# Optimization experiments

Measured on AMD Instinct MI355X. Metric: run time of the kernel, lower is better.

Reference implementation:

```python
import jax, jax.numpy as jnp
import numpy as np

EMBED = 1024
HEADS = 16
HDIM = 64
FFN = 4 * EMBED
EPS = 1e-5


def setup_inputs() -> dict:
    key = jax.random.key(0)
    ks = jax.random.split(key, 12)
    def lin(k, fan_in, shape):
        b = 1.0 / np.sqrt(fan_in)
        return jax.random.uniform(k, shape, jnp.float32, -b, b)
    return {
        "x": jax.random.normal(ks[0], (4, 2048, EMBED), jnp.float32),
        "Wq": lin(ks[1], EMBED, (EMBED, HEADS * HDIM)),
        "Wk": lin(ks[2], EMBED, (EMBED, HEADS * HDIM)),
        "Wv": lin(ks[3], EMBED, (EMBED, HEADS * HDIM)),
        "Wo": lin(ks[4], HEADS * HDIM, (HEADS * HDIM, EMBED)),
        "ln1_g": jnp.ones((EMBED,), jnp.float32),
        "ln1_b": jnp.zeros((EMBED,), jnp.float32),
        "ln2_g": jnp.ones((EMBED,), jnp.float32),
        "ln2_b": jnp.zeros((EMBED,), jnp.float32),
        "W1": lin(ks[5], EMBED, (EMBED, FFN)),
        "b1": lin(ks[6], EMBED, (FFN,)),
        "W2": lin(ks[7], FFN, (FFN, EMBED)),
        "b2": lin(ks[8], FFN, (EMBED,)),
    }


def _layer_norm(x, g, b):
    mu = jnp.mean(x, axis=-1, keepdims=True)
    var = jnp.var(x, axis=-1, keepdims=True)
    return (x - mu) * jax.lax.rsqrt(var + EPS) * g + b


def reference(x, Wq, Wk, Wv, Wo, ln1_g, ln1_b, ln2_g, ln2_b, W1, b1, W2, b2):
    B, S, _ = x.shape
    residual = x
    h = _layer_norm(x, ln1_g, ln1_b)
    # project and split heads: [B, H, S, Dh]
    q = (h @ Wq).reshape(B, S, HEADS, HDIM).transpose(0, 2, 1, 3)
    k = (h @ Wk).reshape(B, S, HEADS, HDIM).transpose(0, 2, 1, 3)
    v = (h @ Wv).reshape(B, S, HEADS, HDIM).transpose(0, 2, 1, 3)
    scale = HDIM ** -0.5
    scores = jnp.einsum("bhqd,bhkd->bhqk", q, k) * scale
    # causal mask (upper triangle excluded above diagonal -> -inf)
    mask = jnp.triu(jnp.ones((S, S), bool), k=1)
    scores = jnp.where(mask, -jnp.inf, scores)
    attn = jax.nn.softmax(scores, axis=-1)
    out = jnp.einsum("bhqk,bhkd->bhqd", attn, v)
    out = out.transpose(0, 2, 1, 3).reshape(B, S, HEADS * HDIM)
    x = residual + out @ Wo
    residual = x
    h = _layer_norm(x, ln2_g, ln2_b)
    h = jax.nn.gelu(h @ W1 + b1, approximate=False) @ W2 + b2
    return residual + h
```

## Files before the change

kernel.cpp:

```cpp
#include <hip/hip_runtime.h>
#include <hip/hip_bf16.h>
#include <math.h>

typedef __bf16 bf16;
typedef bf16 bf16x8 __attribute__((ext_vector_type(8)));
typedef bf16 bf16x4 __attribute__((ext_vector_type(4)));
typedef float f32x4 __attribute__((ext_vector_type(4)));

#define ROWS 8192
#define EMB  1024
#define NH   16
#define HD   64
#define FFN  4096
#define QKVN 3072
#define SEQ  2048

__device__ __forceinline__ void gl2lds16(const bf16* g, bf16* l) {
  __builtin_amdgcn_global_load_lds((const __attribute__((address_space(1))) void*)g,
                                   (__attribute__((address_space(3))) void*)l, 16, 0, 0);
}

__global__ void transpose_cast(const float* __restrict__ W, bf16* __restrict__ Wt,
                               int K, int N, float scale) {
  __shared__ float tile[32][33];
  const int n0 = blockIdx.x * 32, k0 = blockIdx.y * 32;
  const int tx = threadIdx.x & 31, ty = threadIdx.x >> 5;
#pragma unroll
  for (int i = 0; i < 32; i += 8)
    tile[ty + i][tx] = W[(size_t)(k0 + ty + i) * N + n0 + tx];
  __syncthreads();
#pragma unroll
  for (int i = 0; i < 32; i += 8)
    Wt[(size_t)(n0 + ty + i) * K + k0 + tx] = (bf16)(tile[tx][ty + i] * scale);
}

__global__ void v_transpose(const bf16* __restrict__ qkv, bf16* __restrict__ vt) {
  __shared__ bf16 tile[32][33];
  const int s0 = blockIdx.x * 32, d0 = blockIdx.y * 32, bh = blockIdx.z;
  const int b = bh >> 4, h = bh & 15;
  const int tx = threadIdx.x & 31, ty = threadIdx.x >> 5;
#pragma unroll
  for (int i = 0; i < 32; i += 8)
    tile[ty + i][tx] = qkv[(size_t)(b * SEQ + s0 + ty + i) * QKVN + 2 * EMB + h * HD + d0 + tx];
  __syncthreads();
#pragma unroll
  for (int i = 0; i < 32; i += 8)
    vt[(size_t)(bh * HD + d0 + ty + i) * SEQ + s0 + tx] = tile[tx][ty + i];
}

__global__ void layernorm_bf16(const float* __restrict__ x, const float* __restrict__ g,
                               const float* __restrict__ b, bf16* __restrict__ out) {
  const int row = blockIdx.x;
  const int t = threadIdx.x;
  const float4 v = ((const float4*)(x + (size_t)row * EMB))[t];
  float s = v.x + v.y + v.z + v.w;
  float ss = v.x * v.x + v.y * v.y + v.z * v.z + v.w * v.w;
#pragma unroll
  for (int off = 32; off; off >>= 1) {
    s += __shfl_down(s, off);
    ss += __shfl_down(ss, off);
  }
  __shared__ float sbuf[8];
  const int wave = t >> 6, lane = t & 63;
  if (lane == 0) { sbuf[wave] = s; sbuf[4 + wave] = ss; }
  __syncthreads();
  if (t == 0) {
    float S = sbuf[0] + sbuf[1] + sbuf[2] + sbuf[3];
    float SS = sbuf[4] + sbuf[5] + sbuf[6] + sbuf[7];
    float mu = S * (1.0f / EMB);
    float var = SS * (1.0f / EMB) - mu * mu;
    sbuf[0] = mu;
    sbuf[1] = rsqrtf(var + 1e-5f);
  }
  __syncthreads();
  const float mu = sbuf[0], rs = sbuf[1];
  const float4 gv = ((const float4*)g)[t];
  const float4 bv = ((const float4*)b)[t];
  bf16x4 o;
  o[0] = (bf16)((v.x - mu) * rs * gv.x + bv.x);
  o[1] = (bf16)((v.y - mu) * rs * gv.y + bv.y);
  o[2] = (bf16)((v.z - mu) * rs * gv.z + bv.z);
  o[3] = (bf16)((v.w - mu) * rs * gv.w + bv.w);
  *(bf16x4*)(out + (size_t)row * EMB + t * 4) = o;
}

template <int EPI>
__global__ __launch_bounds__(256, 2) void gemm_bt(
    const bf16* __restrict__ A, const bf16* __restrict__ Bt, void* __restrict__ C,
    int M, int N, int K, const float* __restrict__ bias, const float* __restrict__ resid) {
  __shared__ __align__(16) bf16 As[128 * 32];
  __shared__ __align__(16) bf16 Bs[128 * 32];
  const int tid = threadIdx.x;
  const int lane = tid & 63;
  const int wave = tid >> 6;
  const int wm = (wave >> 1) * 64;
  const int wn = (wave & 1) * 64;
  const int m0 = blockIdx.y * 128;
  const int n0 = blockIdx.x * 128;
  const int quad = lane >> 4;
  const int l16 = lane & 15;
  const int k0 = quad * 8;
  const int srow = wave * 32;
  const int lrow = lane >> 2;
  const int lcol = (lane & 3) * 8;

  f32x4 acc[4][4] = {};

  for (int kt = 0; kt < K; kt += 32) {
    __syncthreads();
    gl2lds16(A + (size_t)(m0 + srow + lrow) * K + kt + lcol, &As[srow * 32]);
    gl2lds16(A + (size_t)(m0 + srow + 16 + lrow) * K + kt + lcol, &As[(srow + 16) * 32]);
    gl2lds16(Bt + (size_t)(n0 + srow + lrow) * K + kt + lcol, &Bs[srow * 32]);
    gl2lds16(Bt + (size_t)(n0 + srow + 16 + lrow) * K + kt + lcol, &Bs[(srow + 16) * 32]);
    __syncthreads();
    bf16x8 af[4], bfr[4];
#pragma unroll
    for (int i = 0; i < 4; i++) af[i] = *(const bf16x8*)&As[(wm + i * 16 + l16) * 32 + k0];
#pragma unroll
    for (int j = 0; j < 4; j++) bfr[j] = *(const bf16x8*)&Bs[(wn + j * 16 + l16) * 32 + k0];
#pragma unroll
    for (int i = 0; i < 4; i++)
#pragma unroll
      for (int j = 0; j < 4; j++)
        acc[i][j] = __builtin_amdgcn_mfma_f32_16x16x32_bf16(af[i], bfr[j], acc[i][j], 0, 0, 0);
  }

#pragma unroll
  for (int i = 0; i < 4; i++)
#pragma unroll
    for (int j = 0; j < 4; j++)
#pragma unroll
      for (int r = 0; r < 4; r++) {
        const int row = m0 + wm + i * 16 + quad * 4 + r;
        const int col = n0 + wn + j * 16 + l16;
        const size_t idx = (size_t)row * N + col;
        float v = acc[i][j][r];
        if (EPI == 0) {
          ((bf16*)C)[idx] = (bf16)v;
        } else if (EPI == 1) {
          ((float*)C)[idx] = v + resid[idx];
        } else if (EPI == 2) {
          v += bias[col];
          v = 0.5f * v * (1.0f + erff(v * 0.70710678118654752f));
          ((bf16*)C)[idx] = (bf16)v;
        } else {
          ((float*)C)[idx] = v + bias[col] + resid[idx];
        }
      }
}

__global__ __launch_bounds__(256, 4) void flash_attn(
    const bf16* __restrict__ qkv, const bf16* __restrict__ vt, bf16* __restrict__ out) {
  const int pr = blockIdx.x;
  const int bh = blockIdx.y;
  const int b = bh >> 4, h = bh & 15;
  const int tid = threadIdx.x;
  const int lane = tid & 63, wave = tid >> 6;
  const int quad = lane >> 4, l16 = lane & 15;

  __shared__ __align__(16) bf16 Ks[64][72];
  __shared__ __align__(16) bf16 Vts[64][72];
  __shared__ __align__(16) bf16 Ps[4][16][72];

  const size_t rowbase = (size_t)b * SEQ;
  const int srow = tid >> 3;
  const int sc8 = (tid & 7) * 8;
  const bf16* kbase = qkv + rowbase * QKVN + EMB + h * HD;
  const bf16* vbase = vt + (size_t)(bh * HD) * SEQ;

#pragma unroll 1
  for (int half = 0; half < 2; half++) {
    const int qt = half ? pr : 31 - pr;
    const int qrow_a = qt * 64 + wave * 16 + l16;
    const bf16* qptr = qkv + (rowbase + qrow_a) * QKVN + h * HD;
    const bf16x8 qf0 = *(const bf16x8*)(qptr + quad * 8);
    const bf16x8 qf1 = *(const bf16x8*)(qptr + 32 + quad * 8);
    f32x4 o0 = {}, o1 = {}, o2 = {}, o3 = {};
    f32x4 lsum = {};
    const int qrow_c = qt * 64 + wave * 16 + quad * 4;

#pragma unroll 1
    for (int kt = 0; kt <= qt; kt++) {
      __syncthreads();
      *(bf16x8*)&Ks[srow][sc8] =
          *(const bf16x8*)(kbase + (size_t)(kt * 64 + srow) * QKVN + sc8);
      *(bf16x8*)&Ks[srow + 32][sc8] =
          *(const bf16x8*)(kbase + (size_t)(kt * 64 + srow + 32) * QKVN + sc8);
      *(bf16x8*)&Vts[srow][sc8] =
          *(const bf16x8*)(vbase + (size_t)srow * SEQ + kt * 64 + sc8);
      *(bf16x8*)&Vts[srow + 32][sc8] =
          *(const bf16x8*)(vbase + (size_t)(srow + 32) * SEQ + kt * 64 + sc8);
      __syncthreads();

      if (kt < qt) {
#pragma unroll
        for (int j = 0; j < 4; j++) {
          const bf16x8 kf0 = *(const bf16x8*)&Ks[j * 16 + l16][quad * 8];
          const bf16x8 kf1 = *(const bf16x8*)&Ks[j * 16 + l16][32 + quad * 8];
          f32x4 a = {};
          a = __builtin_amdgcn_mfma_f32_16x16x32_bf16(qf0, kf0, a, 0, 0, 0);
          a = __builtin_amdgcn_mfma_f32_16x16x32_bf16(qf1, kf1, a, 0, 0, 0);
#pragma unroll
          for (int r = 0; r < 4; r++) {
            const float pj = __expf(a[r]);
            lsum[r] += pj;
            Ps[wave][quad * 4 + r][j * 16 + l16] = (bf16)pj;
          }
        }
      } else {
#pragma unroll
        for (int j = 0; j < 4; j++) {
          if (j > wave) {
#pragma unroll
            for (int r = 0; r < 4; r++)
              Ps[wave][quad * 4 + r][j * 16 + l16] = (bf16)0.0f;
          } else {
            const bf16x8 kf0 = *(const bf16x8*)&Ks[j * 16 + l16][quad * 8];
            const bf16x8 kf1 = *(const bf16x8*)&Ks[j * 16 + l16][32 + quad * 8];
            f32x4 a = {};
            a = __builtin_amdgcn_mfma_f32_16x16x32_bf16(qf0, kf0, a, 0, 0, 0);
            a = __builtin_amdgcn_mfma_f32_16x16x32_bf16(qf1, kf1, a, 0, 0, 0);
            if (j == wave) {
#pragma unroll
              for (int r = 0; r < 4; r++) {
                const float v = (l16 > quad * 4 + r) ? -INFINITY : a[r];
                const float pj = __expf(v);
                lsum[r] += pj;
                Ps[wave][quad * 4 + r][j * 16 + l16] = (bf16)pj;
              }
            } else {
#pragma unroll
              for (int r = 0; r < 4; r++) {
                const float pj = __expf(a[r]);
                lsum[r] += pj;
                Ps[wave][quad * 4 + r][j * 16 + l16] = (bf16)pj;
              }
            }
          }
        }
      }

      const bf16x8 af0 = *(const bf16x8*)&Ps[wave][l16][quad * 8];
      const bf16x8 af1 = *(const bf16x8*)&Ps[wave][l16][32 + quad * 8];
      {
        const bf16x8 vf0 = *(const bf16x8*)&Vts[0 + l16][quad * 8];
        const bf16x8 vf1 = *(const bf16x8*)&Vts[0 + l16][32 + quad * 8];
        o0 = __builtin_amdgcn_mfma_f32_16x16x32_bf16(af0, vf0, o0, 0, 0, 0);
        o0 = __builtin_amdgcn_mfma_f32_16x16x32_bf16(af1, vf1, o0, 0, 0, 0);
      }
      {
        const bf16x8 vf0 = *(const bf16x8*)&Vts[16 + l16][quad * 8];
        const bf16x8 vf1 = *(const bf16x8*)&Vts[16 + l16][32 + quad * 8];
        o1 = __builtin_amdgcn_mfma_f32_16x16x32_bf16(af0, vf0, o1, 0, 0, 0);
        o1 = __builtin_amdgcn_mfma_f32_16x16x32_bf16(af1, vf1, o1, 0, 0, 0);
      }
      {
        const bf16x8 vf0 = *(const bf16x8*)&Vts[32 + l16][quad * 8];
        const bf16x8 vf1 = *(const bf16x8*)&Vts[32 + l16][32 + quad * 8];
        o2 = __builtin_amdgcn_mfma_f32_16x16x32_bf16(af0, vf0, o2, 0, 0, 0);
        o2 = __builtin_amdgcn_mfma_f32_16x16x32_bf16(af1, vf1, o2, 0, 0, 0);
      }
      {
        const bf16x8 vf0 = *(const bf16x8*)&Vts[48 + l16][quad * 8];
        const bf16x8 vf1 = *(const bf16x8*)&Vts[48 + l16][32 + quad * 8];
        o3 = __builtin_amdgcn_mfma_f32_16x16x32_bf16(af0, vf0, o3, 0, 0, 0);
        o3 = __builtin_amdgcn_mfma_f32_16x16x32_bf16(af1, vf1, o3, 0, 0, 0);
      }
    }

#pragma unroll
    for (int r = 0; r < 4; r++) {
      float ls = lsum[r];
      ls += __shfl_xor(ls, 1);
      ls += __shfl_xor(ls, 2);
      ls += __shfl_xor(ls, 4);
      ls += __shfl_xor(ls, 8);
      const float iv = 1.0f / ls;
      bf16* op = out + (rowbase + qrow_c + r) * EMB + h * HD;
      op[0 + l16] = (bf16)(o0[r] * iv);
      op[16 + l16] = (bf16)(o1[r] * iv);
      op[32 + l16] = (bf16)(o2[r] * iv);
      op[48 + l16] = (bf16)(o3[r] * iv);
    }
  }
}

extern "C" void kernel_launch(void* const* d_in, const int* in_sizes, int n_in,
                              void* d_out, int out_size, void* d_ws, size_t ws_size,
                              hipStream_t stream) {
  const float* x     = (const float*)d_in[0];
  const float* Wq    = (const float*)d_in[1];
  const float* Wk    = (const float*)d_in[2];
  const float* Wv    = (const float*)d_in[3];
  const float* Wo    = (const float*)d_in[4];
  const float* ln1_g = (const float*)d_in[5];
  const float* ln1_b = (const float*)d_in[6];
  const float* ln2_g = (const float*)d_in[7];
  const float* ln2_b = (const float*)d_in[8];
  const float* W1    = (const float*)d_in[9];
  const float* b1    = (const float*)d_in[10];
  const float* W2    = (const float*)d_in[11];
  const float* b2    = (const float*)d_in[12];
  float* out = (float*)d_out;

  bf16* p = (bf16*)d_ws;
  bf16* wqkv_t = p;                 p += (size_t)QKVN * EMB;
  bf16* wo_t   = p;                 p += (size_t)EMB * EMB;
  bf16* w1_t   = p;                 p += (size_t)FFN * EMB;
  bf16* w2_t   = p;                 p += (size_t)EMB * FFN;
  bf16* h      = p;                 p += (size_t)ROWS * EMB;
  bf16* qkv    = p;                 p += (size_t)ROWS * QKVN;
  bf16* attn_o = p;                 p += (size_t)ROWS * EMB;
  bf16* ffn1   = p;
  bf16* vt     = h;

  transpose_cast<<<dim3(32, 32), 256, 0, stream>>>(Wq, wqkv_t, EMB, EMB, 0.125f);
  transpose_cast<<<dim3(32, 32), 256, 0, stream>>>(Wk, wqkv_t + (size_t)EMB * EMB, EMB, EMB, 1.0f);
  transpose_cast<<<dim3(32, 32), 256, 0, stream>>>(Wv, wqkv_t + (size_t)2 * EMB * EMB, EMB, EMB, 1.0f);
  transpose_cast<<<dim3(32, 32), 256, 0, stream>>>(Wo, wo_t, EMB, EMB, 1.0f);
  transpose_cast<<<dim3(128, 32), 256, 0, stream>>>(W1, w1_t, EMB, FFN, 1.0f);
  transpose_cast<<<dim3(32, 128), 256, 0, stream>>>(W2, w2_t, FFN, EMB, 1.0f);

  layernorm_bf16<<<ROWS, 256, 0, stream>>>(x, ln1_g, ln1_b, h);

  gemm_bt<0><<<dim3(QKVN / 128, ROWS / 128), 256, 0, stream>>>(
      h, wqkv_t, qkv, ROWS, QKVN, EMB, nullptr, nullptr);

  v_transpose<<<dim3(SEQ / 32, HD / 32, 64), 256, 0, stream>>>(qkv, vt);

  flash_attn<<<dim3(16, 64), 256, 0, stream>>>(qkv, vt, attn_o);

  gemm_bt<1><<<dim3(EMB / 128, ROWS / 128), 256, 0, stream>>>(
      attn_o, wo_t, out, ROWS, EMB, EMB, nullptr, x);

  layernorm_bf16<<<ROWS, 256, 0, stream>>>(out, ln2_g, ln2_b, h);

  gemm_bt<2><<<dim3(FFN / 128, ROWS / 128), 256, 0, stream>>>(
      h, w1_t, ffn1, ROWS, FFN, EMB, b1, nullptr);

  gemm_bt<3><<<dim3(EMB / 128, ROWS / 128), 256, 0, stream>>>(
      ffn1, w2_t, out, ROWS, EMB, FFN, b2, out);
}
```

Before: 540.6 us.

## Deepen GEMM K-tile to 64 with XOR-swizzled LDS and grouped block ordering

The bf16 GEMM now stages a K depth of 64 per iteration instead of 32, which halves the number of barrier pairs per tile. The LDS layout uses an XOR swizzle on 16-byte chunks so that the MFMA fragment reads avoid bank conflicts. Blocks are also remapped into groups of 8 along M to improve L2 reuse of the B tiles. LDS use per block doubles, to 32KB, which could reduce occupancy, and M must be a multiple of 8 tiles.

```diff
diff --git a/kernel.cpp b/kernel.cpp
--- a/kernel.cpp
+++ b/kernel.cpp
@@ -88,41 +88,51 @@
 __global__ __launch_bounds__(256, 2) void gemm_bt(
     const bf16* __restrict__ A, const bf16* __restrict__ Bt, void* __restrict__ C,
     int M, int N, int K, const float* __restrict__ bias, const float* __restrict__ resid) {
-  __shared__ __align__(16) bf16 As[128 * 32];
-  __shared__ __align__(16) bf16 Bs[128 * 32];
+  __shared__ __align__(16) bf16 As[128 * 64];
+  __shared__ __align__(16) bf16 Bs[128 * 64];
   const int tid = threadIdx.x;
   const int lane = tid & 63;
   const int wave = tid >> 6;
   const int wm = (wave >> 1) * 64;
   const int wn = (wave & 1) * 64;
-  const int m0 = blockIdx.y * 128;
-  const int n0 = blockIdx.x * 128;
+  const int tn = gridDim.x;
+  const int lin = blockIdx.y * tn + blockIdx.x;
+  const int grp = lin >> 3;
+  const int m0 = ((grp / tn) * 8 + (lin & 7)) * 128;
+  const int n0 = (grp % tn) * 128;
   const int quad = lane >> 4;
   const int l16 = lane & 15;
-  const int k0 = quad * 8;
-  const int srow = wave * 32;
-  const int lrow = lane >> 2;
-  const int lcol = (lane & 3) * 8;
+  const int srow8 = lane >> 3;
+  const int scol = ((lane & 7) ^ srow8) * 8;
+  const int xr = l16 & 7;
 
   f32x4 acc[4][4] = {};
 
-  for (int kt = 0; kt < K; kt += 32) {
+  for (int kt = 0; kt < K; kt += 64) {
     __syncthreads();
-    gl2lds16(A + (size_t)(m0 + srow + lrow) * K + kt + lcol, &As[srow * 32]);
-    gl2lds16(A + (size_t)(m0 + srow + 16 + lrow) * K + kt + lcol, &As[(srow + 16) * 32]);
-    gl2lds16(Bt + (size_t)(n0 + srow + lrow) * K + kt + lcol, &Bs[srow * 32]);
-    gl2lds16(Bt + (size_t)(n0 + srow + 16 + lrow) * K + kt + lcol, &Bs[(srow + 16) * 32]);
+#pragma unroll
+    for (int q = 0; q < 4; q++) {
+      const int br = wave * 32 + q * 8;
+      gl2lds16(A + (size_t)(m0 + br + srow8) * K + kt + scol, &As[br * 64]);
+      gl2lds16(Bt + (size_t)(n0 + br + srow8) * K + kt + scol, &Bs[br * 64]);
+    }
     __syncthreads();
-    bf16x8 af[4], bfr[4];
-#pragma unroll
-    for (int i = 0; i < 4; i++) af[i] = *(const bf16x8*)&As[(wm + i * 16 + l16) * 32 + k0];
-#pragma unroll
-    for (int j = 0; j < 4; j++) bfr[j] = *(const bf16x8*)&Bs[(wn + j * 16 + l16) * 32 + k0];
-#pragma unroll
-    for (int i = 0; i < 4; i++)
+#pragma unroll
+    for (int h = 0; h < 2; h++) {
+      const int cp = ((h * 4 + quad) ^ xr) * 8;
+      bf16x8 af[4], bfr[4];
+#pragma unroll
+      for (int i = 0; i < 4; i++)
+        af[i] = *(const bf16x8*)&As[(wm + i * 16 + l16) * 64 + cp];
 #pragma unroll
       for (int j = 0; j < 4; j++)
-        acc[i][j] = __builtin_amdgcn_mfma_f32_16x16x32_bf16(af[i], bfr[j], acc[i][j], 0, 0, 0);
+        bfr[j] = *(const bf16x8*)&Bs[(wn + j * 16 + l16) * 64 + cp];
+#pragma unroll
+      for (int i = 0; i < 4; i++)
+#pragma unroll
+        for (int j = 0; j < 4; j++)
+          acc[i][j] = __builtin_amdgcn_mfma_f32_16x16x32_bf16(af[i], bfr[j], acc[i][j], 0, 0, 0);
+    }
   }
 
 #pragma unroll
```

After: 509.9 us. 5.7% less time.
